# Performance work log

Measured on AMD Instinct MI355X. Metric: run time of the kernel, lower is better.

Reference implementation:

```python
import jax, jax.numpy as jnp
import numpy as np

COND_DIM = 12 + 12 + 12 + 4 + 4          # 44
VALID_MIDI_COUNT = 128
X_DIM = 2 + VALID_MIDI_COUNT             # 130
HIDDEN = 1024
N_STEP = 16


def _uniform(key, shape, scale):
    return jax.random.uniform(key, shape, jnp.float32, -scale, scale)


def setup_inputs() -> dict:
    key = jax.random.key(0)
    ks = jax.random.split(key, 16)
    B, L = 64, 64                        # batch, length_in_bars
    z = jax.random.normal(ks[0], (B, L, HIDDEN), jnp.float32)
    x = jax.random.normal(ks[1], (B, L * N_STEP, X_DIM + COND_DIM), jnp.float32)
    s = 1.0 / np.sqrt(HIDDEN)
    in0 = X_DIM + COND_DIM               # 174, layer-0 input size
    return {
        "z": z, "x": x,
        "W_ih0": _uniform(ks[2], (4 * HIDDEN, in0), s),
        "W_hh0": _uniform(ks[3], (4 * HIDDEN, HIDDEN), s),
        "b_ih0": _uniform(ks[4], (4 * HIDDEN,), s),
        "b_hh0": _uniform(ks[5], (4 * HIDDEN,), s),
        "W_ih1": _uniform(ks[6], (4 * HIDDEN, HIDDEN), s),
        "W_hh1": _uniform(ks[7], (4 * HIDDEN, HIDDEN), s),
        "b_ih1": _uniform(ks[8], (4 * HIDDEN,), s),
        "b_hh1": _uniform(ks[9], (4 * HIDDEN,), s),
        "Wf": _uniform(ks[10], (X_DIM, HIDDEN), s),
        "bf": _uniform(ks[11], (X_DIM,), s),
    }


def _lstm_cell(inp, h, c, Wih, Whh, bih, bhh):
    # torch LSTMCell gate order: input, forget, cell(g), output
    g = inp @ Wih.T + h @ Whh.T + (bih + bhh)
    i, f, gg, o = jnp.split(g, 4, axis=1)
    c2 = jax.nn.sigmoid(f) * c + jax.nn.sigmoid(i) * jnp.tanh(gg)
    return jax.nn.sigmoid(o) * jnp.tanh(c2), c2


def reference(z, x, W_ih0, W_hh0, b_ih0, b_hh0, W_ih1, W_hh1, b_ih1, b_hh1, Wf, bf):
    B, L, H = z.shape
    Bp = B * L                                   # effective batch
    xr = x.reshape(Bp, N_STEP, x.shape[2])
    zr = z.reshape(Bp, H)
    y = jnp.swapaxes(xr[:, :, -COND_DIM:], 0, 1)  # (16, Bp, COND)

    o0 = jnp.zeros((Bp, X_DIM), z.dtype).at[:, 1].set(1.0)
    c_init = jnp.zeros((Bp, H), z.dtype)

    def step(carry, yt):
        o, h0, c0, h1, c1 = carry
        inp = jnp.concatenate([o, yt], axis=1)
        h0, c0 = _lstm_cell(inp, h0, c0, W_ih0, W_hh0, b_ih0, b_hh0)
        h1, c1 = _lstm_cell(h0, h1, c1, W_ih1, W_hh1, b_ih1, b_hh1)
        logp = jax.nn.log_softmax(h1 @ Wf.T + bf, axis=1)
        # eval-mode hard_max feedback (one-hot of argmax)
        o_next = jax.nn.one_hot(jnp.argmax(logp, axis=1), X_DIM, dtype=logp.dtype)
        return (o_next, h0, c0, h1, c1), logp

    _, logps = jax.lax.scan(step, (o0, zr, c_init, zr, c_init), y)
    # (16, Bp, X_DIM) -> (B, L*16, X_DIM)
    return jnp.swapaxes(logps, 0, 1).reshape(B, L * N_STEP, X_DIM)
```

## Files before the change

kernel.cpp:

```cpp
#include <hip/hip_runtime.h>
#include <hip/hip_bf16.h>

#define HIDDEN   1024
#define XDIM     130
#define CONDDIM  44
#define INDIM    174
#define NSTEP    16
#define BP       4096
#define K0P      1088
#define K1P      2048
#define GN       4096
#define LGN      256
#define SPLITK   16

typedef float f32x4 __attribute__((ext_vector_type(4)));
typedef int   i32x4 __attribute__((ext_vector_type(4)));

__device__ __forceinline__ int fused_row(int n) {
  const int q = (n >> 4) & 3;
  const int j = ((n >> 6) << 4) | (n & 15);
  return q * HIDDEN + j;
}

__device__ __forceinline__ void g2lds16(const void* g, void* l) {
  __builtin_amdgcn_global_load_lds(
      (const __attribute__((address_space(1))) void*)g,
      (__attribute__((address_space(3))) void*)l, 16, 0, 0);
}

__device__ __forceinline__ float sigm(float x)  { return 1.f / (1.f + __expf(-x)); }
__device__ __forceinline__ float tanhfast(float x) { return 2.f / (1.f + __expf(-2.f * x)) - 1.f; }

__device__ __forceinline__ signed char qscale(float v, float inv127s) {
  int q = __float2int_rn(v * inv127s);
  q = q > 127 ? 127 : (q < -127 ? -127 : q);
  return (signed char)q;
}

template<bool FB>
__global__ __launch_bounds__(512, 4)
void gemm_i8_cell_k(const signed char* __restrict__ Alo,
                    const signed char* __restrict__ Ahi, int ahstr,
                    const signed char* __restrict__ W, int K,
                    const float* __restrict__ bcomb,
                    const float* __restrict__ SC,
                    const float* __restrict__ sA,
                    const float* __restrict__ W0T,
                    const int*   __restrict__ idx,
                    float* __restrict__ cT,
                    signed char* __restrict__ d1,
                    signed char* __restrict__ d2,
                    const float* __restrict__ sD2)
{
  __shared__ __align__(16) signed char lds[2 * 24576];

  const int tid  = threadIdx.x;
  const int w    = tid >> 6;
  const int lane = tid & 63;
  const int bid  = blockIdx.x;
  const int xcd  = bid & 7;
  const int rr   = bid >> 3;
  const int mt   = (xcd & 1) * 8 + (rr & 7);
  const int nt   = (xcd >> 1) * 8 + (rr >> 3);
  const int m0   = mt * 256;
  const int n0   = nt * 128;
  const int wm   = w >> 1;
  const int wn   = w & 1;
  const int fr   = lane & 15;
  const int kqs  = (((lane >> 4) ^ ((fr >> 1) & 3)) * 16);
  const int sr   = lane >> 2;
  const int sc   = (((lane & 3) ^ ((sr >> 1) & 3)) * 16);
  const int NT   = K >> 6;

  const int fq = lane >> 4;
  const int cb = n0 + wn * 64;
  const int j  = ((cb >> 6) << 4) | fr;

  i32x4 acc[4][4] = {};

  auto stA = [&](int t, int buf) {
    const signed char* ab; size_t astr; int koff;
    if (t < SPLITK) { ab = Alo; astr = 1024;          koff = t * 64; }
    else            { ab = Ahi; astr = (size_t)ahstr; koff = (t - SPLITK) * 64; }
    #pragma unroll
    for (int i = 0; i < 2; ++i)
      g2lds16(ab + (size_t)(m0 + w * 32 + i * 16 + sr) * astr + (koff + sc),
              (void*)(lds + buf * 24576 + (w * 32 + i * 16) * 64));
  };
  auto stB = [&](int t, int buf) {
    g2lds16(W + (size_t)(n0 + w * 16 + sr) * K + (t * 64 + sc),
            (void*)(lds + buf * 24576 + 16384 + (w * 16) * 64));
  };

  stA(0, 0); stB(0, 0);
  stA(1, 1); stB(1, 1);
  asm volatile("s_waitcnt vmcnt(3)" ::: "memory");
  __builtin_amdgcn_s_barrier();

  for (int t = 0; t < NT; ++t) {
    const int buf = t & 1;
    const signed char* As = lds + buf * 24576;
    const signed char* Bs = As + 16384;

    i32x4 afr[4], bfr[4];
    #pragma unroll
    for (int q = 0; q < 4; ++q)
      afr[q] = *reinterpret_cast<const i32x4*>(&As[(wm * 64 + q * 16 + fr) * 64 + kqs]);
    #pragma unroll
    for (int nf = 0; nf < 4; ++nf)
      bfr[nf] = *reinterpret_cast<const i32x4*>(&Bs[(wn * 64 + nf * 16 + fr) * 64 + kqs]);
    asm volatile("s_waitcnt lgkmcnt(0)" ::: "memory");
    __builtin_amdgcn_s_barrier();
    if (t + 2 < NT) { stA(t + 2, buf); stB(t + 2, buf); }

    __builtin_amdgcn_s_setprio(1);
    #pragma unroll
    for (int q = 0; q < 4; ++q)
      #pragma unroll
      for (int nf = 0; nf < 4; ++nf)
        acc[q][nf] = __builtin_amdgcn_mfma_i32_16x16x64_i8(afr[q], bfr[nf], acc[q][nf], 0, 0, 0);
    __builtin_amdgcn_s_setprio(0);

    if (t + 1 < NT) {
      if (t + 2 < NT) asm volatile("s_waitcnt vmcnt(3)" ::: "memory");
      else            asm volatile("s_waitcnt vmcnt(0)" ::: "memory");
      __builtin_amdgcn_s_barrier();
    }
  }

  const float bs0 = bcomb[cb + fr],      sc0 = SC[cb + fr];
  const float bs1 = bcomb[cb + 16 + fr], sc1 = SC[cb + 16 + fr];
  const float bs2 = bcomb[cb + 32 + fr], sc2 = SC[cb + 32 + fr];
  const float bs3 = bcomb[cb + 48 + fr], sc3 = SC[cb + 48 + fr];
  const size_t ctbase = (size_t)(j >> 5) * ((size_t)BP * 32) + (j & 31);

  #pragma unroll
  for (int mf = 0; mf < 4; ++mf) {
    #pragma unroll
    for (int r = 0; r < 4; ++r) {
      const int b = m0 + wm * 64 + mf * 16 + fq * 4 + r;
      const float sa = sA ? sA[b] : 1.f;
      float gi = (float)acc[mf][0][r] * (sc0 * sa) + bs0;
      float gf = (float)acc[mf][1][r] * (sc1 * sa) + bs1;
      float gg = (float)acc[mf][2][r] * (sc2 * sa) + bs2;
      float go = (float)acc[mf][3][r] * (sc3 * sa) + bs3;
      if (FB) {
        const float* wr = W0T + (size_t)idx[b] * GN;
        gi += wr[cb + fr];
        gf += wr[cb + 16 + fr];
        gg += wr[cb + 32 + fr];
        go += wr[cb + 48 + fr];
      }
      const size_t ci = ctbase + (size_t)b * 32;
      const float cn = sigm(gf) * cT[ci] + sigm(gi) * tanhfast(gg);
      cT[ci] = cn;
      const float hn = sigm(go) * tanhfast(cn);
      d1[(size_t)b * 1024 + j] = qscale(hn, 127.f);
      if (d2) d2[(size_t)b * 1024 + j] = qscale(hn, 127.f / sD2[b]);
    }
  }
}

__global__ __launch_bounds__(256, 4)
void logits_i8_k(const signed char* __restrict__ A, int lda,
                 const signed char* __restrict__ Wfi,
                 const float* __restrict__ SCf,
                 float* __restrict__ C, int ldc)
{
  __shared__ __align__(16) signed char As[64 * 64];
  __shared__ __align__(16) signed char Bs[128 * 64];

  const int tid  = threadIdx.x;
  const int w    = tid >> 6;
  const int lane = tid & 63;
  const int m0 = blockIdx.y * 64;
  const int n0 = blockIdx.x * 128;
  const int wm = w >> 1;
  const int wn = w & 1;
  const int fr = lane & 15;
  const int kqs = (((lane >> 4) ^ ((fr >> 1) & 3)) * 16);
  const int sr  = lane >> 2;
  const int sc  = (((lane & 3) ^ ((sr >> 1) & 3)) * 16);

  i32x4 acc[2][4] = {};

  for (int k0 = 0; k0 < HIDDEN; k0 += 64) {
    __syncthreads();
    g2lds16(A + (size_t)(m0 + w * 16 + sr) * lda + (k0 + sc), (void*)(As + (w * 16) * 64));
    g2lds16(Wfi + (size_t)(n0 + w * 16 + sr) * HIDDEN + (k0 + sc), (void*)(Bs + (w * 16) * 64));
    g2lds16(Wfi + (size_t)(n0 + 64 + w * 16 + sr) * HIDDEN + (k0 + sc), (void*)(Bs + (64 + w * 16) * 64));
    __syncthreads();

    i32x4 af[2], bw[4];
    #pragma unroll
    for (int i = 0; i < 2; ++i)
      af[i] = *reinterpret_cast<const i32x4*>(&As[(wm * 32 + i * 16 + fr) * 64 + kqs]);
    #pragma unroll
    for (int jn = 0; jn < 4; ++jn)
      bw[jn] = *reinterpret_cast<const i32x4*>(&Bs[(wn * 64 + jn * 16 + fr) * 64 + kqs]);
    #pragma unroll
    for (int i = 0; i < 2; ++i)
      #pragma unroll
      for (int jn = 0; jn < 4; ++jn)
        acc[i][jn] = __builtin_amdgcn_mfma_i32_16x16x64_i8(af[i], bw[jn], acc[i][jn], 0, 0, 0);
  }

  const int fq = lane >> 4;
  #pragma unroll
  for (int i = 0; i < 2; ++i)
    #pragma unroll
    for (int jn = 0; jn < 4; ++jn) {
      const int col = n0 + wn * 64 + jn * 16 + fr;
      const float scf = SCf[col];
      #pragma unroll
      for (int r = 0; r < 4; ++r) {
        const int row = m0 + wm * 32 + i * 16 + fq * 4 + r;
        C[(size_t)row * ldc + col] = (float)acc[i][jn][r] * scf;
      }
    }
}

__global__ void smax_k(const float* __restrict__ LG,
                       const float* __restrict__ bfv,
                       float* __restrict__ out, int t,
                       const float* __restrict__ x,
                       signed char* __restrict__ Y,
                       int* __restrict__ idx)
{
  const int b    = blockIdx.x;
  const int lane = threadIdx.x;
  const float NINF = -__builtin_inff();
  const float* lg = LG + (size_t)b * LGN;

  const int c1 = lane + 64, c2 = lane + 128;
  float v0 = lg[lane] + bfv[lane];
  float v1 = lg[c1] + bfv[c1];
  float v2 = (c2 < XDIM) ? lg[c2] + bfv[c2] : NINF;

  float m = fmaxf(v0, fmaxf(v1, v2));
  #pragma unroll
  for (int o = 32; o > 0; o >>= 1) m = fmaxf(m, __shfl_xor(m, o, 64));

  int bi = 0x7fffffff;
  if (v0 == m) bi = lane;
  if (v1 == m) bi = min(bi, c1);
  if (v2 == m) bi = min(bi, c2);
  #pragma unroll
  for (int o = 32; o > 0; o >>= 1) bi = min(bi, __shfl_xor(bi, o, 64));

  float s = __expf(v0 - m) + __expf(v1 - m) + ((c2 < XDIM) ? __expf(v2 - m) : 0.f);
  #pragma unroll
  for (int o = 32; o > 0; o >>= 1) s += __shfl_xor(s, o, 64);
  const float lse = __logf(s);

  float* orow = out + ((size_t)b * NSTEP + t) * XDIM;
  orow[lane] = v0 - m - lse;
  orow[c1]   = v1 - m - lse;
  if (c2 < XDIM) orow[c2] = v2 - m - lse;
  if (lane == 0) idx[b] = bi;

  if (t + 1 < NSTEP) {
    const float yv = (lane < CONDDIM)
        ? x[((size_t)b * NSTEP + (t + 1)) * INDIM + XDIM + lane] : 0.f;
    Y[(size_t)b * 64 + lane] = qscale(yv * 0.25f, 127.f);
  }
}

__global__ void initq_k(const float* __restrict__ z, const float* __restrict__ x,
                        float* __restrict__ c0T, float* __restrict__ c1T,
                        signed char* __restrict__ Hz0,
                        signed char* __restrict__ Hz1,
                        signed char* __restrict__ Y,
                        float* __restrict__ S0, float* __restrict__ S1,
                        int* __restrict__ idx)
{
  const int b    = blockIdx.x;
  const int lane = threadIdx.x;
  const float* zr = z + (size_t)b * HIDDEN;

  float mz = 0.f;
  for (int k = lane; k < HIDDEN; k += 64) mz = fmaxf(mz, fabsf(zr[k]));
  #pragma unroll
  for (int o = 32; o > 0; o >>= 1) mz = fmaxf(mz, __shfl_xor(mz, o, 64));

  const float yv = (lane < CONDDIM) ? x[((size_t)b * NSTEP) * INDIM + XDIM + lane] : 0.f;
  float my = fabsf(yv) * 0.25f;
  #pragma unroll
  for (int o = 32; o > 0; o >>= 1) my = fmaxf(my, __shfl_xor(my, o, 64));

  const float s0 = fmaxf(fmaxf(mz, my), 1e-6f);
  const float s1 = fmaxf(mz, 1.f);
  const float i0 = 127.f / s0;
  const float i1 = 127.f / s1;

  for (int k = lane; k < HIDDEN; k += 64) {
    const float zv = zr[k];
    Hz0[(size_t)b * 1024 + k] = qscale(zv, i0);
    Hz1[(size_t)b * 1024 + k] = qscale(zv, i1);
    const size_t ci = (size_t)(k >> 5) * ((size_t)BP * 32) + (size_t)b * 32 + (k & 31);
    c0T[ci] = 0.f;
    c1T[ci] = 0.f;
  }
  Y[(size_t)b * 64 + lane] = qscale(yv * 0.25f, i0);
  if (lane == 0) { S0[b] = s0; S1[b] = s1; idx[b] = 1; }
}

__global__ void rowmax0_k(const float* __restrict__ Wih0, const float* __restrict__ Whh0,
                          float* __restrict__ RM, float* __restrict__ SC)
{
  const int n = blockIdx.x, lane = threadIdx.x;
  const int row = fused_row(n);
  float m = 1e-20f;
  for (int k = lane; k < HIDDEN; k += 64)  m = fmaxf(m, fabsf(Whh0[(size_t)row * HIDDEN + k]));
  for (int k = lane; k < CONDDIM; k += 64) m = fmaxf(m, 4.f * fabsf(Wih0[(size_t)row * INDIM + XDIM + k]));
  #pragma unroll
  for (int o = 32; o > 0; o >>= 1) m = fmaxf(m, __shfl_xor(m, o, 64));
  if (lane == 0) { RM[n] = m; SC[n] = m / 16129.f; }
}

__global__ void rowmax1_k(const float* __restrict__ Wih1, const float* __restrict__ Whh1,
                          float* __restrict__ RM, float* __restrict__ SC)
{
  const int n = blockIdx.x, lane = threadIdx.x;
  const int row = fused_row(n);
  float m = 1e-20f;
  for (int k = lane; k < HIDDEN; k += 64) {
    m = fmaxf(m, fabsf(Wih1[(size_t)row * HIDDEN + k]));
    m = fmaxf(m, fabsf(Whh1[(size_t)row * HIDDEN + k]));
  }
  #pragma unroll
  for (int o = 32; o > 0; o >>= 1) m = fmaxf(m, __shfl_xor(m, o, 64));
  if (lane == 0) { RM[n] = m; SC[n] = m / 16129.f; }
}

__global__ void packi0_k(const float* __restrict__ Wih0, const float* __restrict__ Whh0,
                         const float* __restrict__ RM, signed char* __restrict__ Bp)
{
  const int t = blockIdx.x * blockDim.x + threadIdx.x;
  if (t >= GN * K0P) return;
  const int n = t / K0P, k = t % K0P;
  const int row = fused_row(n);
  float v = 0.f;
  if (k < HIDDEN)                v = Whh0[(size_t)row * HIDDEN + k];
  else if (k < HIDDEN + CONDDIM) v = 4.f * Wih0[(size_t)row * INDIM + XDIM + (k - HIDDEN)];
  Bp[t] = qscale(v, 127.f / RM[n]);
}

__global__ void packi1_k(const float* __restrict__ Wih1, const float* __restrict__ Whh1,
                         const float* __restrict__ RM, signed char* __restrict__ Bp)
{
  const int t = blockIdx.x * blockDim.x + threadIdx.x;
  if (t >= GN * K1P) return;
  const int n = t >> 11, k = t & 2047;
  const int row = fused_row(n);
  const float v = (k < HIDDEN) ? Wih1[(size_t)row * HIDDEN + k]
                               : Whh1[(size_t)row * HIDDEN + (k - HIDDEN)];
  Bp[t] = qscale(v, 127.f / RM[n]);
}

__global__ void packbias_k(const float* __restrict__ bih, const float* __restrict__ bhh,
                           float* __restrict__ bc)
{
  const int n = blockIdx.x * blockDim.x + threadIdx.x;
  if (n >= GN) return;
  const int row = fused_row(n);
  bc[n] = bih[row] + bhh[row];
}

__global__ void rowmaxf_k(const float* __restrict__ Wf, float* __restrict__ RM,
                          float* __restrict__ SC)
{
  const int n = blockIdx.x, lane = threadIdx.x;
  float m = 1e-20f;
  if (n < XDIM)
    for (int k = lane; k < HIDDEN; k += 64) m = fmaxf(m, fabsf(Wf[(size_t)n * HIDDEN + k]));
  else m = 1.f;
  #pragma unroll
  for (int o = 32; o > 0; o >>= 1) m = fmaxf(m, __shfl_xor(m, o, 64));
  if (lane == 0) { RM[n] = m; SC[n] = m / 16129.f; }
}

__global__ void packfi_k(const float* __restrict__ Wf, const float* __restrict__ RM,
                         signed char* __restrict__ Wfi)
{
  const int t = blockIdx.x * blockDim.x + threadIdx.x;
  if (t >= LGN * HIDDEN) return;
  const int r = t >> 10, k = t & 1023;
  const float v = (r < XDIM) ? Wf[(size_t)r * HIDDEN + k] : 0.f;
  Wfi[t] = qscale(v, 127.f / RM[r]);
}

__global__ void packt_k(const float* __restrict__ Wih0, float* __restrict__ W0T)
{
  const int t = blockIdx.x * blockDim.x + threadIdx.x;
  if (t >= XDIM * GN) return;
  const int e = t >> 12, n = t & 4095;
  W0T[t] = Wih0[(size_t)fused_row(n) * INDIM + e];
}

extern "C" void kernel_launch(void* const* d_in, const int* in_sizes, int n_in,
                              void* d_out, int out_size, void* d_ws, size_t ws_size,
                              hipStream_t stream)
{
  const float* z    = (const float*)d_in[0];
  const float* x    = (const float*)d_in[1];
  const float* Wih0 = (const float*)d_in[2];
  const float* Whh0 = (const float*)d_in[3];
  const float* bih0 = (const float*)d_in[4];
  const float* bhh0 = (const float*)d_in[5];
  const float* Wih1 = (const float*)d_in[6];
  const float* Whh1 = (const float*)d_in[7];
  const float* bih1 = (const float*)d_in[8];
  const float* bhh1 = (const float*)d_in[9];
  const float* Wf   = (const float*)d_in[10];
  const float* bfv  = (const float*)d_in[11];
  float* out = (float*)d_out;

  char* ws = (char*)d_ws;
  size_t off = 0;
  auto alloc = [&](size_t bytes) { void* p = ws + off; off += (bytes + 255) & ~(size_t)255; return p; };

  float*       LG   = (float*)      alloc((size_t)BP * LGN * 4);
  signed char* H0a  = (signed char*)alloc((size_t)BP * 1024);
  signed char* H0b  = (signed char*)alloc((size_t)BP * 1024);
  signed char* H0s1 = (signed char*)alloc((size_t)BP * 1024);
  signed char* H1a  = (signed char*)alloc((size_t)BP * 1024);
  signed char* H1b  = (signed char*)alloc((size_t)BP * 1024);
  signed char* Y    = (signed char*)alloc((size_t)BP * 64);
  signed char* Bpi0 = (signed char*)alloc((size_t)GN * K0P);
  signed char* Bpi1 = (signed char*)alloc((size_t)GN * K1P);
  signed char* Wfi  = (signed char*)alloc((size_t)LGN * HIDDEN);
  float*       W0T  = (float*)      alloc((size_t)XDIM * GN * 4);
  float*       bc0  = (float*)      alloc((size_t)GN * 4);
  float*       bc1  = (float*)      alloc((size_t)GN * 4);
  float*       RM0  = (float*)      alloc((size_t)GN * 4);
  float*       SC0  = (float*)      alloc((size_t)GN * 4);
  float*       RM1  = (float*)      alloc((size_t)GN * 4);
  float*       SC1  = (float*)      alloc((size_t)GN * 4);
  float*       RMf  = (float*)      alloc((size_t)LGN * 4);
  float*       SCf  = (float*)      alloc((size_t)LGN * 4);
  float*       S0   = (float*)      alloc((size_t)BP * 4);
  float*       S1   = (float*)      alloc((size_t)BP * 4);
  float*       c0T  = (float*)      alloc((size_t)BP * HIDDEN * 4);
  float*       c1T  = (float*)      alloc((size_t)BP * HIDDEN * 4);
  int*         idx  = (int*)        alloc((size_t)BP * 4);
  (void)ws_size; (void)in_sizes; (void)n_in; (void)out_size;

  rowmax0_k<<<GN, 64, 0, stream>>>(Wih0, Whh0, RM0, SC0);
  rowmax1_k<<<GN, 64, 0, stream>>>(Wih1, Whh1, RM1, SC1);
  rowmaxf_k<<<LGN, 64, 0, stream>>>(Wf, RMf, SCf);
  packi0_k<<<(GN * K0P + 255) / 256, 256, 0, stream>>>(Wih0, Whh0, RM0, Bpi0);
  packi1_k<<<(GN * K1P + 255) / 256, 256, 0, stream>>>(Wih1, Whh1, RM1, Bpi1);
  packfi_k<<<(LGN * HIDDEN + 255) / 256, 256, 0, stream>>>(Wf, RMf, Wfi);
  packbias_k<<<(GN + 255) / 256, 256, 0, stream>>>(bih0, bhh0, bc0);
  packbias_k<<<(GN + 255) / 256, 256, 0, stream>>>(bih1, bhh1, bc1);
  packt_k<<<(XDIM * GN + 255) / 256, 256, 0, stream>>>(Wih0, W0T);
  initq_k<<<BP, 64, 0, stream>>>(z, x, c0T, c1T, H0b, H1b, Y, S0, S1, idx);

  for (int t = 0; t < NSTEP; ++t) {
    signed char* H0cur  = (t & 1) ? H0b : H0a;
    signed char* H0prev = (t & 1) ? H0a : H0b;
    signed char* H1cur  = (t & 1) ? H1b : H1a;
    signed char* H1prev = (t & 1) ? H1a : H1b;

    gemm_i8_cell_k<true><<<512, 512, 0, stream>>>(
        H0prev, Y, 64, Bpi0, K0P, bc0, SC0,
        (t == 0) ? S0 : nullptr, W0T, idx, c0T,
        H0cur,
        (t == 0) ? H0s1 : nullptr, S1);
    gemm_i8_cell_k<false><<<512, 512, 0, stream>>>(
        (t == 0) ? H0s1 : H0cur, H1prev, 1024, Bpi1, K1P, bc1, SC1,
        (t == 0) ? S1 : nullptr, nullptr, nullptr, c1T,
        H1cur, nullptr, nullptr);
    logits_i8_k<<<dim3(LGN / 128, BP / 64), dim3(256), 0, stream>>>(
        H1cur, 1024, Wfi, SCf, LG, LGN);
    smax_k<<<BP, 64, 0, stream>>>(LG, bfv, out, t, x, Y, idx);
  }
}
```

Baseline: 1.580 ms.

## Triple-buffer LDS in int8 GEMM to drop per-iteration read barrier

The int8 MFMA GEMM now keeps three LDS stage buffers instead of two, so the prefetch for tile t+2 writes to a buffer nobody is reading. That removes the mid-loop lgkmcnt wait and barrier that guarded the buffer reuse, and the prefetch is issued before the fragment loads. Per-thread global base pointers are also precomputed to cut address math in the stage function. In exchange LDS use per block goes from 48KB to 72KB, which may lower occupancy under the 4-blocks-per-CU launch bound.

```diff
diff --git a/kernel.cpp b/kernel.cpp
--- a/kernel.cpp
+++ b/kernel.cpp
@@ -52,7 +52,7 @@
                     signed char* __restrict__ d2,
                     const float* __restrict__ sD2)
 {
-  __shared__ __align__(16) signed char lds[2 * 24576];
+  __shared__ __align__(16) signed char lds[3 * 24576];
 
   const int tid  = threadIdx.x;
   const int w    = tid >> 6;
@@ -78,29 +78,35 @@
 
   i32x4 acc[4][4] = {};
 
-  auto stA = [&](int t, int buf) {
-    const signed char* ab; size_t astr; int koff;
-    if (t < SPLITK) { ab = Alo; astr = 1024;          koff = t * 64; }
-    else            { ab = Ahi; astr = (size_t)ahstr; koff = (t - SPLITK) * 64; }
-    #pragma unroll
-    for (int i = 0; i < 2; ++i)
-      g2lds16(ab + (size_t)(m0 + w * 32 + i * 16 + sr) * astr + (koff + sc),
-              (void*)(lds + buf * 24576 + (w * 32 + i * 16) * 64));
+  const signed char* aLo0 = Alo + (size_t)(m0 + w * 32 +      sr) * 1024  + sc;
+  const signed char* aLo1 = Alo + (size_t)(m0 + w * 32 + 16 + sr) * 1024  + sc;
+  const signed char* aHi0 = Ahi + (size_t)(m0 + w * 32 +      sr) * ahstr + sc;
+  const signed char* aHi1 = Ahi + (size_t)(m0 + w * 32 + 16 + sr) * ahstr + sc;
+  const signed char* bB   = W   + (size_t)(n0 + w * 16 +      sr) * K     + sc;
+
+  auto stage = [&](int t, int buf) {
+    signed char* dA = lds + buf * 24576 + (w * 32) * 64;
+    signed char* dB = lds + buf * 24576 + 16384 + (w * 16) * 64;
+    const bool lo = t < SPLITK;
+    const signed char* s0 = lo ? aLo0 : aHi0;
+    const signed char* s1 = lo ? aLo1 : aHi1;
+    const int ko = (lo ? t : t - SPLITK) * 64;
+    g2lds16(s0 + ko, dA);
+    g2lds16(s1 + ko, dA + 1024);
+    g2lds16(bB + t * 64, dB);
   };
-  auto stB = [&](int t, int buf) {
-    g2lds16(W + (size_t)(n0 + w * 16 + sr) * K + (t * 64 + sc),
-            (void*)(lds + buf * 24576 + 16384 + (w * 16) * 64));
-  };
-
-  stA(0, 0); stB(0, 0);
-  stA(1, 1); stB(1, 1);
+
+  stage(0, 0);
+  stage(1, 1);
   asm volatile("s_waitcnt vmcnt(3)" ::: "memory");
   __builtin_amdgcn_s_barrier();
 
+  int bcur = 0, bnx2 = 2;
   for (int t = 0; t < NT; ++t) {
-    const int buf = t & 1;
-    const signed char* As = lds + buf * 24576;
+    const signed char* As = lds + bcur * 24576;
     const signed char* Bs = As + 16384;
+
+    if (t + 2 < NT) stage(t + 2, bnx2);
 
     i32x4 afr[4], bfr[4];
     #pragma unroll
@@ -109,9 +115,6 @@
     #pragma unroll
     for (int nf = 0; nf < 4; ++nf)
       bfr[nf] = *reinterpret_cast<const i32x4*>(&Bs[(wn * 64 + nf * 16 + fr) * 64 + kqs]);
-    asm volatile("s_waitcnt lgkmcnt(0)" ::: "memory");
-    __builtin_amdgcn_s_barrier();
-    if (t + 2 < NT) { stA(t + 2, buf); stB(t + 2, buf); }
 
     __builtin_amdgcn_s_setprio(1);
     #pragma unroll
@@ -126,6 +129,8 @@
       else            asm volatile("s_waitcnt vmcnt(0)" ::: "memory");
       __builtin_amdgcn_s_barrier();
     }
+    bcur = (bcur == 2) ? 0 : bcur + 1;
+    bnx2 = (bnx2 == 2) ? 0 : bnx2 + 1;
   }
 
   const float bs0 = bcomb[cb + fr],      sc0 = SC[cb + fr];
```

Measured after the change: 1.563 ms (median of 2 runs). Within noise of the previous version (-1.1%).
